# Performance work log

Hardware: AMD Instinct MI355X
Metric: run time of the kernel (lower is better)

## Reference

```python
import jax, jax.numpy as jnp
import numpy as np

C, B, N, IN, OUT = 32, 32, 4096, 16, 32
NUM_ITERS = 3


def _squash(t, axis=-1):
    # scale = |t|^2 / (1 + |t|^2); out = scale * t / |t|
    sn = jnp.sum(t * t, axis=axis, keepdims=True)
    return (sn / (1.0 + sn)) * t / jnp.sqrt(sn)


def setup_inputs() -> dict:
    key = jax.random.key(0)
    k1, k2 = jax.random.split(key)
    x = jax.random.normal(k1, (B, N, IN), dtype=jnp.float32)
    route_weights = jax.random.normal(k2, (C, N, IN, OUT), dtype=jnp.float32)
    return {"x": x, "route_weights": route_weights}


def reference(x, route_weights):
    # priors[c,b,n,d] = sum_i x[b,n,i] * W[c,n,i,d]  (torch: [C,B,N,1,D], singleton dropped)
    priors = jnp.einsum('bni,cnio->cbno', x, route_weights)  # [C,B,N,D]
    # torch logits are [C,B,N,1,D] but constant over D (delta broadcasts), and the
    # custom softmax normalizes over dim=2 (route nodes N), so [C,B,N] is equivalent.
    logits = jnp.zeros(priors.shape[:3], dtype=priors.dtype)  # [C,B,N]
    outputs = None
    for i in range(NUM_ITERS):
        probs = jax.nn.softmax(logits, axis=2)  # softmax over route nodes (dim=2)
        s = jnp.sum(probs[..., None] * priors, axis=2, keepdims=True)  # [C,B,1,D]
        outputs = _squash(s, axis=-1)
        if i != NUM_ITERS - 1:
            logits = logits + jnp.sum(priors * outputs, axis=-1)  # agreement [C,B,N]
    return outputs[:, :, :, None, :]  # [C,B,1,1,D] to match torch output shape
```

## Files before the change

kernel.cpp:

```cpp
#include <hip/hip_runtime.h>
#include <math.h>


typedef _Float16 f16x8 __attribute__((ext_vector_type(8)));
typedef float f32x16 __attribute__((ext_vector_type(16)));

namespace {
constexpr int kC = 32, kB = 32, kN = 4096, kI = 16, kD = 32;
constexpr int CHUNKS = 32;
constexpr int CHUNK_N = kN / CHUNKS;
constexpr int PS = kB * kD + kB;
constexpr int GRID = kC * CHUNKS;
constexpr size_t XT_ELEMS = (size_t)kN * kB * kI;
constexpr size_t WT_ELEMS = (size_t)kC * kN * kI * kD;
constexpr size_t P_FLOATS = (size_t)kC * CHUNKS * PS;
constexpr size_t CV_FLOATS = (size_t)kC * kB * kD;
constexpr int BAR_U32 = 33;
constexpr size_t WS_BYTES_MID = XT_ELEMS * 2 + (P_FLOATS + CV_FLOATS) * 4;
constexpr size_t WS_BYTES_BIG =
    (XT_ELEMS + WT_ELEMS) * 2 + (P_FLOATS + CV_FLOATS) * 4;
constexpr size_t WS_BYTES_MEGA =
    (XT_ELEMS + WT_ELEMS) * 2 + 3 * P_FLOATS * 4 + 256;
}

__device__ __forceinline__ f32x16 zero16() {
  f32x16 z;
#pragma unroll
  for (int r = 0; r < 16; ++r) z[r] = 0.f;
  return z;
}

__global__ __launch_bounds__(256) void k_xt(const float* __restrict__ x,
                                            _Float16* __restrict__ xt,
                                            unsigned* __restrict__ bar) {
  if (bar && blockIdx.x == 0 && threadIdx.x < BAR_U32) bar[threadIdx.x] = 0u;
  const int t = blockIdx.x * 256 + threadIdx.x;
  const int r = t >> 1, half = t & 1;
  const int b = r >> 12, n = r & 4095;
  const float4* s4 =
      reinterpret_cast<const float4*>(x) + (size_t)r * 4 + half * 2;
  const float4 f0 = s4[0], f1 = s4[1];
  f16x8 o;
  o[0] = (_Float16)f0.x; o[1] = (_Float16)f0.y;
  o[2] = (_Float16)f0.z; o[3] = (_Float16)f0.w;
  o[4] = (_Float16)f1.x; o[5] = (_Float16)f1.y;
  o[6] = (_Float16)f1.z; o[7] = (_Float16)f1.w;
  *reinterpret_cast<f16x8*>(xt + ((size_t)n * kB + b) * kI + half * 8) = o;
}

__device__ __forceinline__ void bar_arrive(unsigned* bar, int bid, int tid) {
  __threadfence();
  __syncthreads();
  if (tid == 0) {
    const int g = bid & 31;
    unsigned v = __hip_atomic_fetch_add(&bar[g], 1u, __ATOMIC_RELEASE,
                                        __HIP_MEMORY_SCOPE_AGENT);
    if ((v & 31u) == 31u)
      __hip_atomic_fetch_add(&bar[32], 1u, __ATOMIC_RELEASE,
                             __HIP_MEMORY_SCOPE_AGENT);
  }
}

__device__ __forceinline__ void bar_wait(unsigned* bar, int tid, int epoch) {
  if (tid == 0) {
    const unsigned target = 32u * (unsigned)epoch;
    while (__hip_atomic_load(&bar[32], __ATOMIC_RELAXED,
                             __HIP_MEMORY_SCOPE_AGENT) < target)
      __builtin_amdgcn_s_sleep(8);
    (void)__hip_atomic_load(&bar[32], __ATOMIC_ACQUIRE,
                            __HIP_MEMORY_SCOPE_AGENT);
  }
  __syncthreads();
}


__device__ __forceinline__ void mega_sweep0(const float* __restrict__ W,
                                            const _Float16* __restrict__ xt,
                                            _Float16* __restrict__ Wt,
                                            float* __restrict__ P,
                                            float (*red)[32][33], int c,
                                            int chunk, int tid) {
  const int w = tid >> 6, l = tid & 63;
  const int m = l & 31, h = l >> 5;
  const int n0 = chunk * CHUNK_N;
  constexpr int TILES = CHUNK_N / 4;

  const float* wp = W + ((size_t)c * kN + n0 + w) * 512 + (h * 8) * 32 + m;
  const _Float16* xp = xt + ((size_t)(n0 + w)) * 512 + m * 16 + h * 8;
  _Float16* wtp = Wt + ((size_t)c * kN + n0 + w) * 512 + (size_t)l * 8;

  f32x16 accA = zero16(), accB = zero16();

  float rA0[8], rA1[8];
  f16x8 B0, B1;
#pragma unroll
  for (int j = 0; j < 8; ++j) rA0[j] = __builtin_nontemporal_load(wp + j * 32);
  B0 = *reinterpret_cast<const f16x8*>(xp);
#pragma unroll
  for (int j = 0; j < 8; ++j)
    rA1[j] = __builtin_nontemporal_load(wp + 2048 + j * 32);
  B1 = *reinterpret_cast<const f16x8*>(xp + 2048);

#pragma unroll 1
  for (int t = 0; t < TILES; t += 2) {
    {
      f16x8 a;
#pragma unroll
      for (int j = 0; j < 8; ++j) a[j] = (_Float16)rA0[j];
      const f16x8 b = B0;
      const int tn = (t + 2 < TILES) ? t + 2 : 0;
#pragma unroll
      for (int j = 0; j < 8; ++j)
        rA0[j] = __builtin_nontemporal_load(wp + (size_t)tn * 2048 + j * 32);
      B0 = *reinterpret_cast<const f16x8*>(xp + (size_t)tn * 2048);
      *reinterpret_cast<f16x8*>(wtp + (size_t)t * 2048) = a;
      accA = __builtin_amdgcn_mfma_f32_32x32x16_f16(a, b, accA, 0, 0, 0);
    }
    {
      f16x8 a;
#pragma unroll
      for (int j = 0; j < 8; ++j) a[j] = (_Float16)rA1[j];
      const f16x8 b = B1;
      const int tn = (t + 3 < TILES) ? t + 3 : 0;
#pragma unroll
      for (int j = 0; j < 8; ++j)
        rA1[j] = __builtin_nontemporal_load(wp + (size_t)tn * 2048 + j * 32);
      B1 = *reinterpret_cast<const f16x8*>(xp + (size_t)tn * 2048);
      *reinterpret_cast<f16x8*>(wtp + (size_t)(t + 1) * 2048) = a;
      accB = __builtin_amdgcn_mfma_f32_32x32x16_f16(a, b, accB, 0, 0, 0);
    }
  }
#pragma unroll
  for (int r = 0; r < 16; ++r) accA[r] += accB[r];

#pragma unroll
  for (int r = 0; r < 16; ++r)
    red[w][(r & 3) + 8 * (r >> 2) + 4 * h][m] = accA[r];
  __syncthreads();

  float* Pp = P + ((size_t)c * CHUNKS + chunk) * PS;
#pragma unroll
  for (int e = tid; e < 1024; e += 256) {
    const int d = e >> 5, bb = e & 31;
    Pp[e] = red[0][d][bb] + red[1][d][bb] + red[2][d][bb] + red[3][d][bb];
  }
}

__device__ __forceinline__ void mega_sweep_wt(
    const _Float16* __restrict__ Wt, const _Float16* __restrict__ xt,
    const float (*sCV)[32], float* __restrict__ P, float (*red)[32][33],
    float (*lred)[32], int c, int chunk, int tid) {
  const int w = tid >> 6, l = tid & 63;
  const int m = l & 31, h = l >> 5;
  const int n0 = chunk * CHUNK_N;
  constexpr int TILES = CHUNK_N / 4;

  const _Float16* wp = Wt + ((size_t)c * kN + n0 + w) * 512 + (size_t)l * 8;
  const _Float16* xp = xt + ((size_t)(n0 + w)) * 512 + m * 16 + h * 8;

  float cvr[16];
#pragma unroll
  for (int r = 0; r < 16; ++r)
    cvr[r] = sCV[m][(r & 3) + 8 * (r >> 2) + 4 * h];

  f32x16 accA = zero16(), accB = zero16();
  float lacc = 0.f;
  const f32x16 z = zero16();

  f16x8 A0, A1, B0, B1;
  A0 = *reinterpret_cast<const f16x8*>(wp);
  B0 = *reinterpret_cast<const f16x8*>(xp);
  A1 = *reinterpret_cast<const f16x8*>(wp + 2048);
  B1 = *reinterpret_cast<const f16x8*>(xp + 2048);

#pragma unroll 1
  for (int t = 0; t < TILES; t += 2) {
    {
      const f16x8 a = A0;
      const f16x8 b = B0;
      const int tn = (t + 2 < TILES) ? t + 2 : 0;
      A0 = *reinterpret_cast<const f16x8*>(wp + (size_t)tn * 2048);
      B0 = *reinterpret_cast<const f16x8*>(xp + (size_t)tn * 2048);
      const f32x16 pr =
          __builtin_amdgcn_mfma_f32_32x32x16_f16(a, b, z, 0, 0, 0);
      float d0 = pr[0] * cvr[0], d1 = pr[1] * cvr[1];
      float d2 = pr[2] * cvr[2], d3 = pr[3] * cvr[3];
#pragma unroll
      for (int r = 4; r < 16; r += 4) {
        d0 = fmaf(pr[r + 0], cvr[r + 0], d0);
        d1 = fmaf(pr[r + 1], cvr[r + 1], d1);
        d2 = fmaf(pr[r + 2], cvr[r + 2], d2);
        d3 = fmaf(pr[r + 3], cvr[r + 3], d3);
      }
      float dp = (d0 + d1) + (d2 + d3);
      dp += __shfl_xor(dp, 32);
      const float e = __expf(dp);
      lacc += e;
#pragma unroll
      for (int r = 0; r < 16; ++r) accA[r] = fmaf(e, pr[r], accA[r]);
    }
    {
      const f16x8 a = A1;
      const f16x8 b = B1;
      const int tn = (t + 3 < TILES) ? t + 3 : 0;
      A1 = *reinterpret_cast<const f16x8*>(wp + (size_t)tn * 2048);
      B1 = *reinterpret_cast<const f16x8*>(xp + (size_t)tn * 2048);
      const f32x16 pr =
          __builtin_amdgcn_mfma_f32_32x32x16_f16(a, b, z, 0, 0, 0);
      float d0 = pr[0] * cvr[0], d1 = pr[1] * cvr[1];
      float d2 = pr[2] * cvr[2], d3 = pr[3] * cvr[3];
#pragma unroll
      for (int r = 4; r < 16; r += 4) {
        d0 = fmaf(pr[r + 0], cvr[r + 0], d0);
        d1 = fmaf(pr[r + 1], cvr[r + 1], d1);
        d2 = fmaf(pr[r + 2], cvr[r + 2], d2);
        d3 = fmaf(pr[r + 3], cvr[r + 3], d3);
      }
      float dp = (d0 + d1) + (d2 + d3);
      dp += __shfl_xor(dp, 32);
      const float e = __expf(dp);
      lacc += e;
#pragma unroll
      for (int r = 0; r < 16; ++r) accB[r] = fmaf(e, pr[r], accB[r]);
    }
  }
#pragma unroll
  for (int r = 0; r < 16; ++r) accA[r] += accB[r];

#pragma unroll
  for (int r = 0; r < 16; ++r)
    red[w][(r & 3) + 8 * (r >> 2) + 4 * h][m] = accA[r];
  if (h == 0) lred[w][m] = lacc;
  __syncthreads();

  float* Pp = P + ((size_t)c * CHUNKS + chunk) * PS;
#pragma unroll
  for (int e = tid; e < 1024; e += 256) {
    const int d = e >> 5, bb = e & 31;
    Pp[e] = red[0][d][bb] + red[1][d][bb] + red[2][d][bb] + red[3][d][bb];
  }
  if (tid < 32)
    Pp[1024 + tid] = lred[0][tid] + lred[1][tid] + lred[2][tid] + lred[3][tid];
}

template <int K>
__device__ __forceinline__ void mega_reduce(const float* __restrict__ P,
                                            float* __restrict__ out,
                                            float (&cvrun)[4],
                                            float (*sCV)[32], int c, int t) {
  const int b = t >> 3, dg = t & 7;
  const float* Pc = P + (size_t)c * CHUNKS * PS;
  float s0 = 0.f, s1 = 0.f, s2 = 0.f, s3 = 0.f, lb = 0.f;
#pragma unroll 4
  for (int ch = 0; ch < CHUNKS; ++ch) {
    const float* base = Pc + (size_t)ch * PS;
    s0 += __hip_atomic_load(base + (dg + 0) * 32 + b, __ATOMIC_RELAXED,
                            __HIP_MEMORY_SCOPE_AGENT);
    s1 += __hip_atomic_load(base + (dg + 8) * 32 + b, __ATOMIC_RELAXED,
                            __HIP_MEMORY_SCOPE_AGENT);
    s2 += __hip_atomic_load(base + (dg + 16) * 32 + b, __ATOMIC_RELAXED,
                            __HIP_MEMORY_SCOPE_AGENT);
    s3 += __hip_atomic_load(base + (dg + 24) * 32 + b, __ATOMIC_RELAXED,
                            __HIP_MEMORY_SCOPE_AGENT);
    if (K != 0 && dg == 0)
      lb += __hip_atomic_load(base + 1024 + b, __ATOMIC_RELAXED,
                              __HIP_MEMORY_SCOPE_AGENT);
  }
  float inv;
  if constexpr (K == 0) {
    inv = 1.0f / (float)kN;
  } else {
    lb = __shfl(lb, (t & 63) & 56);
    inv = 1.0f / lb;
  }
  const float v0 = s0 * inv, v1 = s1 * inv, v2 = s2 * inv, v3 = s3 * inv;
  float sn = v0 * v0 + v1 * v1 + v2 * v2 + v3 * v3;
  sn += __shfl_xor(sn, 1);
  sn += __shfl_xor(sn, 2);
  sn += __shfl_xor(sn, 4);
  const float coef = sqrtf(sn) / (1.0f + sn);
  if constexpr (K == 2) {
    const size_t o0 = (size_t)c * 1024 + b * 32 + dg;
    out[o0 + 0] = v0 * coef;  out[o0 + 8] = v1 * coef;
    out[o0 + 16] = v2 * coef; out[o0 + 24] = v3 * coef;
  } else {
    if constexpr (K == 0) {
      cvrun[0] = v0 * coef; cvrun[1] = v1 * coef;
      cvrun[2] = v2 * coef; cvrun[3] = v3 * coef;
    } else {
      cvrun[0] += v0 * coef; cvrun[1] += v1 * coef;
      cvrun[2] += v2 * coef; cvrun[3] += v3 * coef;
    }
    sCV[b][dg + 0] = cvrun[0];  sCV[b][dg + 8] = cvrun[1];
    sCV[b][dg + 16] = cvrun[2]; sCV[b][dg + 24] = cvrun[3];
  }
}

__global__ __launch_bounds__(256, 4) void k_mega2(
    const float* __restrict__ W, const _Float16* __restrict__ xt,
    _Float16* __restrict__ Wt, float* __restrict__ P0, float* __restrict__ P1,
    float* __restrict__ P2, unsigned* __restrict__ bar,
    float* __restrict__ out) {
  __shared__ float red[4][32][33];
  __shared__ float lred[4][32];
  __shared__ float sCV[32][32];
  const int bid = blockIdx.x;
  const int c = bid & 31;
  const int chunk = bid >> 5;
  const int tid = threadIdx.x;
  float cvrun[4] = {0.f, 0.f, 0.f, 0.f};

  mega_sweep0(W, xt, Wt, P0, red, c, chunk, tid);
  bar_arrive(bar, bid, tid);
  bar_wait(bar, tid, 1);

  mega_reduce<0>(P0, nullptr, cvrun, sCV, c, tid);
  __syncthreads();

  mega_sweep_wt(Wt, xt, sCV, P1, red, lred, c, chunk, tid);
  bar_arrive(bar, bid, tid);
  bar_wait(bar, tid, 2);

  mega_reduce<1>(P1, nullptr, cvrun, sCV, c, tid);
  __syncthreads();

  mega_sweep_wt(Wt, xt, sCV, P2, red, lred, c, chunk, tid);
  bar_arrive(bar, bid, tid);

  if (chunk == 0) {
    bar_wait(bar, tid, 3);
    mega_reduce<2>(P2, out, cvrun, sCV, c, tid);
  }
}


template <int MODE, bool EMIT>
__global__ __launch_bounds__(256) void k_sweep(const float* __restrict__ W,
                                               const _Float16* __restrict__ xt,
                                               const float* __restrict__ cumVec,
                                               float* __restrict__ partials,
                                               _Float16* __restrict__ Wt) {
  __shared__ float red[4][32][33];
  __shared__ float lred[4][32];
  const int bid = blockIdx.x;
  const int c = bid & 31;
  const int chunk = bid >> 5;
  const int tid = threadIdx.x;
  const int w = tid >> 6, l = tid & 63;
  const int m = l & 31, h = l >> 5;
  const int n0 = chunk * CHUNK_N;
  constexpr int TILES = CHUNK_N / 4;

  const float* wp = W + ((size_t)c * kN + n0 + w) * 512 + (h * 8) * 32 + m;
  const _Float16* xp = xt + ((size_t)(n0 + w)) * 512 + m * 16 + h * 8;
  _Float16* wtp =
      EMIT ? (Wt + ((size_t)c * kN + n0 + w) * 512 + (size_t)l * 8) : nullptr;

  float cvr[16];
  if (MODE) {
    const float* cvp = cumVec + (size_t)c * 1024 + m * 32;
#pragma unroll
    for (int r = 0; r < 16; ++r) cvr[r] = cvp[(r & 3) + 8 * (r >> 2) + 4 * h];
  }

  f32x16 accA = zero16(), accB = zero16();
  float lacc = 0.f;
  const f32x16 z = zero16();

  float rA0[8], rA1[8];
  f16x8 B0, B1;
#pragma unroll
  for (int j = 0; j < 8; ++j)
    rA0[j] = EMIT ? __builtin_nontemporal_load(wp + j * 32) : wp[j * 32];
  B0 = *reinterpret_cast<const f16x8*>(xp);
#pragma unroll
  for (int j = 0; j < 8; ++j)
    rA1[j] = EMIT ? __builtin_nontemporal_load(wp + 2048 + j * 32)
                  : wp[2048 + j * 32];
  B1 = *reinterpret_cast<const f16x8*>(xp + 2048);

#pragma unroll 1
  for (int t = 0; t < TILES; t += 2) {
    {
      f16x8 a;
#pragma unroll
      for (int j = 0; j < 8; ++j) a[j] = (_Float16)rA0[j];
      const f16x8 b = B0;
      const int tn = (t + 2 < TILES) ? t + 2 : 0;
#pragma unroll
      for (int j = 0; j < 8; ++j)
        rA0[j] = EMIT ? __builtin_nontemporal_load(wp + (size_t)tn * 2048 +
                                                   j * 32)
                      : wp[(size_t)tn * 2048 + j * 32];
      B0 = *reinterpret_cast<const f16x8*>(xp + (size_t)tn * 2048);
      if constexpr (EMIT)
        *reinterpret_cast<f16x8*>(wtp + (size_t)t * 2048) = a;
      if constexpr (MODE == 0) {
        accA = __builtin_amdgcn_mfma_f32_32x32x16_f16(a, b, accA, 0, 0, 0);
      } else {
        const f32x16 pr =
            __builtin_amdgcn_mfma_f32_32x32x16_f16(a, b, z, 0, 0, 0);
        float d0 = pr[0] * cvr[0], d1 = pr[1] * cvr[1];
        float d2 = pr[2] * cvr[2], d3 = pr[3] * cvr[3];
#pragma unroll
        for (int r = 4; r < 16; r += 4) {
          d0 = fmaf(pr[r + 0], cvr[r + 0], d0);
          d1 = fmaf(pr[r + 1], cvr[r + 1], d1);
          d2 = fmaf(pr[r + 2], cvr[r + 2], d2);
          d3 = fmaf(pr[r + 3], cvr[r + 3], d3);
        }
        float dp = (d0 + d1) + (d2 + d3);
        dp += __shfl_xor(dp, 32);
        const float e = __expf(dp);
        lacc += e;
#pragma unroll
        for (int r = 0; r < 16; ++r) accA[r] = fmaf(e, pr[r], accA[r]);
      }
    }
    {
      f16x8 a;
#pragma unroll
      for (int j = 0; j < 8; ++j) a[j] = (_Float16)rA1[j];
      const f16x8 b = B1;
      const int tn = (t + 3 < TILES) ? t + 3 : 0;
#pragma unroll
      for (int j = 0; j < 8; ++j)
        rA1[j] = EMIT ? __builtin_nontemporal_load(wp + (size_t)tn * 2048 +
                                                   j * 32)
                      : wp[(size_t)tn * 2048 + j * 32];
      B1 = *reinterpret_cast<const f16x8*>(xp + (size_t)tn * 2048);
      if constexpr (EMIT)
        *reinterpret_cast<f16x8*>(wtp + (size_t)(t + 1) * 2048) = a;
      if constexpr (MODE == 0) {
        accB = __builtin_amdgcn_mfma_f32_32x32x16_f16(a, b, accB, 0, 0, 0);
      } else {
        const f32x16 pr =
            __builtin_amdgcn_mfma_f32_32x32x16_f16(a, b, z, 0, 0, 0);
        float d0 = pr[0] * cvr[0], d1 = pr[1] * cvr[1];
        float d2 = pr[2] * cvr[2], d3 = pr[3] * cvr[3];
#pragma unroll
        for (int r = 4; r < 16; r += 4) {
          d0 = fmaf(pr[r + 0], cvr[r + 0], d0);
          d1 = fmaf(pr[r + 1], cvr[r + 1], d1);
          d2 = fmaf(pr[r + 2], cvr[r + 2], d2);
          d3 = fmaf(pr[r + 3], cvr[r + 3], d3);
        }
        float dp = (d0 + d1) + (d2 + d3);
        dp += __shfl_xor(dp, 32);
        const float e = __expf(dp);
        lacc += e;
#pragma unroll
        for (int r = 0; r < 16; ++r) accB[r] = fmaf(e, pr[r], accB[r]);
      }
    }
  }
#pragma unroll
  for (int r = 0; r < 16; ++r) accA[r] += accB[r];

#pragma unroll
  for (int r = 0; r < 16; ++r)
    red[w][(r & 3) + 8 * (r >> 2) + 4 * h][m] = accA[r];
  if (MODE && h == 0) lred[w][m] = lacc;
  __syncthreads();

  float* Pp = partials + ((size_t)c * CHUNKS + chunk) * PS;
#pragma unroll
  for (int e = tid; e < 1024; e += 256) {
    const int d = e >> 5, bb = e & 31;
    Pp[e] = red[0][d][bb] + red[1][d][bb] + red[2][d][bb] + red[3][d][bb];
  }
  if (MODE && tid < 32)
    Pp[1024 + tid] = lred[0][tid] + lred[1][tid] + lred[2][tid] + lred[3][tid];
}

__global__ __launch_bounds__(256) void k_sweep_wt(
    const _Float16* __restrict__ Wt, const _Float16* __restrict__ xt,
    const float* __restrict__ cumVec, float* __restrict__ partials) {
  __shared__ float red[4][32][33];
  __shared__ float lred[4][32];
  __shared__ float sCV[32][32];
  const int bid = blockIdx.x;
  const int c = bid & 31;
  const int chunk = bid >> 5;
  const int tid = threadIdx.x;
  for (int e = tid; e < 1024; e += 256)
    sCV[e >> 5][e & 31] = cumVec[(size_t)c * 1024 + e];
  __syncthreads();
  mega_sweep_wt(Wt, xt, sCV, partials, red, lred, c, chunk, tid);
}

template <int K>
__global__ __launch_bounds__(1024) void k_reduce(
    const float* __restrict__ partials, float* __restrict__ CV,
    float* __restrict__ out) {
  const int c = blockIdx.x;
  const int t = threadIdx.x;
  const int b = t >> 5, d = t & 31;
  const float* Pc = partials + (size_t)c * CHUNKS * PS;
  float s = 0.f;
#pragma unroll 4
  for (int ch = 0; ch < CHUNKS; ++ch) s += Pc[(size_t)ch * PS + d * 32 + b];
  float inv;
  if constexpr (K == 0) {
    inv = 1.0f / (float)kN;
  } else {
    float lb = 0.f;
#pragma unroll 4
    for (int ch = 0; ch < CHUNKS; ++ch) lb += Pc[(size_t)ch * PS + 1024 + b];
    inv = 1.0f / lb;
  }
  const float sv = s * inv;
  float sn = sv * sv;
  sn += __shfl_xor(sn, 1);
  sn += __shfl_xor(sn, 2);
  sn += __shfl_xor(sn, 4);
  sn += __shfl_xor(sn, 8);
  sn += __shfl_xor(sn, 16);
  const float coef = sqrtf(sn) / (1.0f + sn);
  const float o = sv * coef;
  if constexpr (K == 2)
    out[(size_t)c * 1024 + t] = o;
  else if constexpr (K == 0)
    CV[(size_t)c * 1024 + t] = o;
  else
    CV[(size_t)c * 1024 + t] += o;
}

namespace v1 {
constexpr int BG = 4, NSLOT = 128, THREADS1 = NSLOT * 8;
template <int MODE>
__device__ __forceinline__ void sweep_pass(const float* __restrict__ Wc,
                                           const float* __restrict__ x, int b0,
                                           int tid, int nslot, int dg,
                                           float (*red)[8][20], float (*sS)[kD],
                                           float* sL, const float (*sVec)[kD]) {
  float acc[BG][4];
  float lv[BG];
#pragma unroll
  for (int b = 0; b < BG; ++b) {
    lv[b] = 0.f;
#pragma unroll
    for (int j = 0; j < 4; ++j) acc[b][j] = 0.f;
  }
  float vec[BG][4];
  if (MODE) {
#pragma unroll
    for (int b = 0; b < BG; ++b)
#pragma unroll
      for (int j = 0; j < 4; ++j) vec[b][j] = sVec[b][4 * dg + j];
  }
#pragma unroll 1
  for (int n = nslot; n < kN; n += NSLOT) {
    const float* Wn = Wc + (size_t)n * (kI * kD) + 4 * dg;
    float pr[BG][4];
#pragma unroll
    for (int b = 0; b < BG; ++b)
#pragma unroll
      for (int j = 0; j < 4; ++j) pr[b][j] = 0.f;
#pragma unroll
    for (int iq = 0; iq < 4; ++iq) {
      float4 wv[4];
#pragma unroll
      for (int r = 0; r < 4; ++r)
        wv[r] = *reinterpret_cast<const float4*>(Wn + (4 * iq + r) * kD);
#pragma unroll
      for (int b = 0; b < BG; ++b) {
        const float4 xv = *reinterpret_cast<const float4*>(
            x + ((size_t)(b0 + b) * kN + n) * kI + 4 * iq);
        const float xsv[4] = {xv.x, xv.y, xv.z, xv.w};
#pragma unroll
        for (int r = 0; r < 4; ++r) {
          pr[b][0] = fmaf(xsv[r], wv[r].x, pr[b][0]);
          pr[b][1] = fmaf(xsv[r], wv[r].y, pr[b][1]);
          pr[b][2] = fmaf(xsv[r], wv[r].z, pr[b][2]);
          pr[b][3] = fmaf(xsv[r], wv[r].w, pr[b][3]);
        }
      }
    }
    if (MODE == 0) {
#pragma unroll
      for (int b = 0; b < BG; ++b)
#pragma unroll
        for (int j = 0; j < 4; ++j) acc[b][j] += pr[b][j];
    } else {
#pragma unroll
      for (int b = 0; b < BG; ++b) {
        float dp = pr[b][0] * vec[b][0] + pr[b][1] * vec[b][1] +
                   pr[b][2] * vec[b][2] + pr[b][3] * vec[b][3];
        dp += __shfl_xor(dp, 1);
        dp += __shfl_xor(dp, 2);
        dp += __shfl_xor(dp, 4);
        const float e = __expf(dp);
        lv[b] += e;
        acc[b][0] = fmaf(e, pr[b][0], acc[b][0]);
        acc[b][1] = fmaf(e, pr[b][1], acc[b][1]);
        acc[b][2] = fmaf(e, pr[b][2], acc[b][2]);
        acc[b][3] = fmaf(e, pr[b][3], acc[b][3]);
      }
    }
  }
#pragma unroll
  for (int b = 0; b < BG; ++b) {
#pragma unroll
    for (int j = 0; j < 4; ++j) {
      float v = acc[b][j];
      v += __shfl_xor(v, 8);
      v += __shfl_xor(v, 16);
      v += __shfl_xor(v, 32);
      acc[b][j] = v;
    }
    if (MODE) {
      float v = lv[b];
      v += __shfl_xor(v, 8);
      v += __shfl_xor(v, 16);
      v += __shfl_xor(v, 32);
      lv[b] = v;
    }
  }
  const int lane = tid & 63;
  const int wv_id = tid >> 6;
  if ((lane >> 3) == 0) {
#pragma unroll
    for (int b = 0; b < BG; ++b) {
#pragma unroll
      for (int j = 0; j < 4; ++j) red[wv_id][dg][4 * b + j] = acc[b][j];
      if (MODE) red[wv_id][dg][16 + b] = lv[b];
    }
  }
  __syncthreads();
  if (tid < 128) {
    const int dgc = tid >> 4, e = tid & 15;
    float s = 0.f;
#pragma unroll
    for (int w = 0; w < 16; ++w) s += red[w][dgc][e];
    sS[e >> 2][4 * dgc + (e & 3)] = s;
  }
  if (MODE && tid >= 128 && tid < 128 + BG) {
    const int b = tid - 128;
    float s = 0.f;
#pragma unroll
    for (int w = 0; w < 16; ++w) s += red[w][0][16 + b];
    sL[b] = s;
  }
  __syncthreads();
}

__global__ __launch_bounds__(THREADS1, 4) void caps_route_kernel(
    const float* __restrict__ x, const float* __restrict__ W,
    float* __restrict__ out) {
  __shared__ float red[16][8][20];
  __shared__ float sS[BG][kD];
  __shared__ float sVec[BG][kD];
  __shared__ float sL[BG];
  const int i = blockIdx.x;
  const int xcd = i & 7;
  const int j = i >> 3;
  const int c = xcd + 8 * (j >> 3);
  const int b0 = 4 * (j & 7);
  const int tid = threadIdx.x;
  const int nslot = tid >> 3;
  const int dg = tid & 7;
  const float* Wc = W + (size_t)c * kN * kI * kD;
  sweep_pass<0>(Wc, x, b0, tid, nslot, dg, red, sS, sL, sVec);
  if (tid < BG) {
    const int b = tid;
    float sval[kD], sn = 0.f;
    const float inv = 1.0f / (float)kN;
#pragma unroll
    for (int d = 0; d < kD; ++d) {
      sval[d] = sS[b][d] * inv;
      sn += sval[d] * sval[d];
    }
    const float coef = sqrtf(sn) / (1.0f + sn);
#pragma unroll
    for (int d = 0; d < kD; ++d) sVec[b][d] = sval[d] * coef;
  }
  __syncthreads();
  sweep_pass<1>(Wc, x, b0, tid, nslot, dg, red, sS, sL, sVec);
  if (tid < BG) {
    const int b = tid;
    float sval[kD], sn = 0.f;
    const float inv = 1.0f / sL[b];
#pragma unroll
    for (int d = 0; d < kD; ++d) {
      sval[d] = sS[b][d] * inv;
      sn += sval[d] * sval[d];
    }
    const float coef = sqrtf(sn) / (1.0f + sn);
#pragma unroll
    for (int d = 0; d < kD; ++d) sVec[b][d] += sval[d] * coef;
  }
  __syncthreads();
  sweep_pass<1>(Wc, x, b0, tid, nslot, dg, red, sS, sL, sVec);
  if (tid < BG) {
    const int b = tid;
    float sval[kD], sn = 0.f;
    const float inv = 1.0f / sL[b];
#pragma unroll
    for (int d = 0; d < kD; ++d) {
      sval[d] = sS[b][d] * inv;
      sn += sval[d] * sval[d];
    }
    const float coef = sqrtf(sn) / (1.0f + sn);
    float* o = out + ((size_t)c * kB + (b0 + b)) * kD;
#pragma unroll
    for (int d = 0; d < kD; ++d) o[d] = sval[d] * coef;
  }
}
}

namespace {
int g_mega_ok = 0;
int probe_mega() {
  int dev = 0;
  if (hipGetDevice(&dev) != hipSuccess) return 0;
  int nCU = 0;
  if (hipDeviceGetAttribute(&nCU, hipDeviceAttributeMultiprocessorCount,
                            dev) != hipSuccess)
    return 0;
  int maxB = 0;
  if (hipOccupancyMaxActiveBlocksPerMultiprocessor(&maxB, k_mega2, 256, 0) !=
      hipSuccess)
    return 0;
  return (nCU > 0 && maxB > 0 && (size_t)nCU * (size_t)maxB >= (size_t)GRID)
             ? 1
             : -1;
}
struct MegaProbeInit {
  MegaProbeInit() { g_mega_ok = probe_mega(); }
} g_mega_probe_init;
}

extern "C" void kernel_launch(void* const* d_in, const int* in_sizes, int n_in,
                              void* d_out, int out_size, void* d_ws,
                              size_t ws_size, hipStream_t stream) {
  const float* x = (const float*)d_in[0];
  const float* W = (const float*)d_in[1];
  float* out = (float*)d_out;
  (void)in_sizes; (void)n_in; (void)out_size;

  if (g_mega_ok == 0) g_mega_ok = probe_mega();

  if (g_mega_ok == 1 && ws_size >= WS_BYTES_MEGA) {
    _Float16* xt = (_Float16*)d_ws;
    _Float16* Wt = xt + XT_ELEMS;
    float* P0 = (float*)(Wt + WT_ELEMS);
    float* P1 = P0 + P_FLOATS;
    float* P2 = P1 + P_FLOATS;
    unsigned* bar = (unsigned*)(P2 + P_FLOATS);

    k_xt<<<GRID, 256, 0, stream>>>(x, xt, bar);
    k_mega2<<<GRID, 256, 0, stream>>>(W, xt, Wt, P0, P1, P2, bar, out);
    return;
  }

  if (ws_size >= WS_BYTES_BIG) {
    _Float16* xt = (_Float16*)d_ws;
    _Float16* Wt = xt + XT_ELEMS;
    float* P = (float*)(Wt + WT_ELEMS);
    float* CV = P + P_FLOATS;

    k_xt<<<GRID, 256, 0, stream>>>(x, xt, nullptr);
    k_sweep<0, true><<<GRID, 256, 0, stream>>>(W, xt, nullptr, P, Wt);
    k_reduce<0><<<kC, 1024, 0, stream>>>(P, CV, nullptr);
    k_sweep_wt<<<GRID, 256, 0, stream>>>(Wt, xt, CV, P);
    k_reduce<1><<<kC, 1024, 0, stream>>>(P, CV, nullptr);
    k_sweep_wt<<<GRID, 256, 0, stream>>>(Wt, xt, CV, P);
    k_reduce<2><<<kC, 1024, 0, stream>>>(P, nullptr, out);
    return;
  }

  if (ws_size >= WS_BYTES_MID) {
    _Float16* xt = (_Float16*)d_ws;
    float* P = (float*)(xt + XT_ELEMS);
    float* CV = P + P_FLOATS;

    k_xt<<<GRID, 256, 0, stream>>>(x, xt, nullptr);
    k_sweep<0, false><<<GRID, 256, 0, stream>>>(W, xt, nullptr, P, nullptr);
    k_reduce<0><<<kC, 1024, 0, stream>>>(P, CV, nullptr);
    k_sweep<1, false><<<GRID, 256, 0, stream>>>(W, xt, CV, P, nullptr);
    k_reduce<1><<<kC, 1024, 0, stream>>>(P, CV, nullptr);
    k_sweep<1, false><<<GRID, 256, 0, stream>>>(W, xt, CV, P, nullptr);
    k_reduce<2><<<kC, 1024, 0, stream>>>(P, nullptr, out);
    return;
  }

  v1::caps_route_kernel<<<256, v1::THREADS1, 0, stream>>>(x, W, out);
}
```

Baseline: 200.7 us.

## Replace grid-wide barrier with per-capsule group barriers and a single reducer block

The grid-wide two-level barrier is replaced by a per-output-capsule counter, so only the 32 blocks sharing a capsule wait for each other. One block per group (chunk 0) reduces the partials, writes the running output vector to global memory and raises a flag that the other blocks spin on before loading it into shared memory. The three partial buffers collapse into one reused buffer, and the reduction uses 64-bit loads with an LDS-based norm reduction. The cost is a serialized reduce-then-broadcast step per iteration instead of every block reducing redundantly, plus an extra flag round trip. The fast path now also runs when the occupancy probe fails, which risks deadlock if blocks are not all co-resident.

After: 200.8 us. About the same (+0.1%).

```diff
diff --git a/kernel.cpp b/kernel.cpp
--- a/kernel.cpp
+++ b/kernel.cpp
@@ -15,12 +15,12 @@
 constexpr size_t WT_ELEMS = (size_t)kC * kN * kI * kD;
 constexpr size_t P_FLOATS = (size_t)kC * CHUNKS * PS;
 constexpr size_t CV_FLOATS = (size_t)kC * kB * kD;
-constexpr int BAR_U32 = 33;
+constexpr int BAR_U32 = 2048;
 constexpr size_t WS_BYTES_MID = XT_ELEMS * 2 + (P_FLOATS + CV_FLOATS) * 4;
 constexpr size_t WS_BYTES_BIG =
     (XT_ELEMS + WT_ELEMS) * 2 + (P_FLOATS + CV_FLOATS) * 4;
 constexpr size_t WS_BYTES_MEGA =
-    (XT_ELEMS + WT_ELEMS) * 2 + 3 * P_FLOATS * 4 + 256;
+    (XT_ELEMS + WT_ELEMS) * 2 + (P_FLOATS + CV_FLOATS) * 4 + BAR_U32 * 4 + 256;
 }
 
 __device__ __forceinline__ f32x16 zero16() {
@@ -33,7 +33,8 @@
 __global__ __launch_bounds__(256) void k_xt(const float* __restrict__ x,
                                             _Float16* __restrict__ xt,
                                             unsigned* __restrict__ bar) {
-  if (bar && blockIdx.x == 0 && threadIdx.x < BAR_U32) bar[threadIdx.x] = 0u;
+  if (bar && blockIdx.x == 0)
+    for (int i = threadIdx.x; i < BAR_U32; i += 256) bar[i] = 0u;
   const int t = blockIdx.x * 256 + threadIdx.x;
   const int r = t >> 1, half = t & 1;
   const int b = r >> 12, n = r & 4095;
@@ -48,29 +49,26 @@
   *reinterpret_cast<f16x8*>(xt + ((size_t)n * kB + b) * kI + half * 8) = o;
 }
 
-__device__ __forceinline__ void bar_arrive(unsigned* bar, int bid, int tid) {
+__device__ __forceinline__ void group_arrive(unsigned* ctr, int tid) {
   __threadfence();
   __syncthreads();
-  if (tid == 0) {
-    const int g = bid & 31;
-    unsigned v = __hip_atomic_fetch_add(&bar[g], 1u, __ATOMIC_RELEASE,
-                                        __HIP_MEMORY_SCOPE_AGENT);
-    if ((v & 31u) == 31u)
-      __hip_atomic_fetch_add(&bar[32], 1u, __ATOMIC_RELEASE,
-                             __HIP_MEMORY_SCOPE_AGENT);
-  }
-}
-
-__device__ __forceinline__ void bar_wait(unsigned* bar, int tid, int epoch) {
-  if (tid == 0) {
-    const unsigned target = 32u * (unsigned)epoch;
-    while (__hip_atomic_load(&bar[32], __ATOMIC_RELAXED,
-                             __HIP_MEMORY_SCOPE_AGENT) < target)
-      __builtin_amdgcn_s_sleep(8);
-    (void)__hip_atomic_load(&bar[32], __ATOMIC_ACQUIRE,
-                            __HIP_MEMORY_SCOPE_AGENT);
-  }
-  __syncthreads();
+  if (tid == 0)
+    __hip_atomic_fetch_add(ctr, 1u, __ATOMIC_RELEASE,
+                           __HIP_MEMORY_SCOPE_AGENT);
+}
+
+__device__ __forceinline__ void spin_ge(unsigned* addr, unsigned target) {
+  while (__hip_atomic_load(addr, __ATOMIC_RELAXED,
+                           __HIP_MEMORY_SCOPE_AGENT) < target)
+    __builtin_amdgcn_s_sleep(2);
+}
+
+__device__ __forceinline__ float ld_f32_agent(const float* p) {
+  return __hip_atomic_load(p, __ATOMIC_RELAXED, __HIP_MEMORY_SCOPE_AGENT);
+}
+__device__ __forceinline__ unsigned long long ld_u64_agent(const float* p) {
+  return __hip_atomic_load(reinterpret_cast<const unsigned long long*>(p),
+                           __ATOMIC_RELAXED, __HIP_MEMORY_SCOPE_AGENT);
 }
 
 
@@ -244,92 +242,154 @@
 }
 
 template <int K>
-__device__ __forceinline__ void mega_reduce(const float* __restrict__ P,
-                                            float* __restrict__ out,
-                                            float (&cvrun)[4],
-                                            float (*sCV)[32], int c, int t) {
-  const int b = t >> 3, dg = t & 7;
+__device__ __forceinline__ void red_reduce(const float* __restrict__ P,
+                                           float* __restrict__ CVc,
+                                           float* __restrict__ out,
+                                           float (&cvrun)[4],
+                                           float (*ldsSn)[16][2],
+                                           float* ldsCoef, float* ldsInv,
+                                           int c, int tid) {
   const float* Pc = P + (size_t)c * CHUNKS * PS;
-  float s0 = 0.f, s1 = 0.f, s2 = 0.f, s3 = 0.f, lb = 0.f;
+  const int hb = tid & 15;
+  const int b0 = hb * 2;
+  const int d0 = tid >> 4;
+  float s0 = 0.f, s1 = 0.f, s2 = 0.f, s3 = 0.f;
 #pragma unroll 4
   for (int ch = 0; ch < CHUNKS; ++ch) {
     const float* base = Pc + (size_t)ch * PS;
-    s0 += __hip_atomic_load(base + (dg + 0) * 32 + b, __ATOMIC_RELAXED,
-                            __HIP_MEMORY_SCOPE_AGENT);
-    s1 += __hip_atomic_load(base + (dg + 8) * 32 + b, __ATOMIC_RELAXED,
-                            __HIP_MEMORY_SCOPE_AGENT);
-    s2 += __hip_atomic_load(base + (dg + 16) * 32 + b, __ATOMIC_RELAXED,
-                            __HIP_MEMORY_SCOPE_AGENT);
-    s3 += __hip_atomic_load(base + (dg + 24) * 32 + b, __ATOMIC_RELAXED,
-                            __HIP_MEMORY_SCOPE_AGENT);
-    if (K != 0 && dg == 0)
-      lb += __hip_atomic_load(base + 1024 + b, __ATOMIC_RELAXED,
-                              __HIP_MEMORY_SCOPE_AGENT);
-  }
-  float inv;
+    const unsigned long long q0 = ld_u64_agent(base + 2 * tid);
+    const unsigned long long q1 = ld_u64_agent(base + 512 + 2 * tid);
+    s0 += __uint_as_float((unsigned)q0);
+    s1 += __uint_as_float((unsigned)(q0 >> 32));
+    s2 += __uint_as_float((unsigned)q1);
+    s3 += __uint_as_float((unsigned)(q1 >> 32));
+  }
+  float inv0, inv1;
   if constexpr (K == 0) {
-    inv = 1.0f / (float)kN;
+    inv0 = inv1 = 1.0f / (float)kN;
   } else {
-    lb = __shfl(lb, (t & 63) & 56);
-    inv = 1.0f / lb;
-  }
-  const float v0 = s0 * inv, v1 = s1 * inv, v2 = s2 * inv, v3 = s3 * inv;
-  float sn = v0 * v0 + v1 * v1 + v2 * v2 + v3 * v3;
-  sn += __shfl_xor(sn, 1);
-  sn += __shfl_xor(sn, 2);
-  sn += __shfl_xor(sn, 4);
-  const float coef = sqrtf(sn) / (1.0f + sn);
+    if (tid < 32) {
+      float lb = 0.f;
+#pragma unroll 4
+      for (int ch = 0; ch < CHUNKS; ++ch)
+        lb += ld_f32_agent(Pc + (size_t)ch * PS + 1024 + tid);
+      ldsInv[tid] = 1.0f / lb;
+    }
+    __syncthreads();
+    inv0 = ldsInv[b0];
+    inv1 = ldsInv[b0 + 1];
+  }
+  const float v0 = s0 * inv0, v1 = s1 * inv1;
+  const float v2 = s2 * inv0, v3 = s3 * inv1;
+  float snA = v0 * v0 + v2 * v2;
+  float snB = v1 * v1 + v3 * v3;
+  snA += __shfl_xor(snA, 16); snA += __shfl_xor(snA, 32);
+  snB += __shfl_xor(snB, 16); snB += __shfl_xor(snB, 32);
+  if ((tid & 63) < 16) {
+    ldsSn[tid >> 6][hb][0] = snA;
+    ldsSn[tid >> 6][hb][1] = snB;
+  }
+  __syncthreads();
+  if (tid < 16) {
+    const float sA = ldsSn[0][tid][0] + ldsSn[1][tid][0] + ldsSn[2][tid][0] +
+                     ldsSn[3][tid][0];
+    const float sB = ldsSn[0][tid][1] + ldsSn[1][tid][1] + ldsSn[2][tid][1] +
+                     ldsSn[3][tid][1];
+    ldsCoef[2 * tid] = sqrtf(sA) / (1.0f + sA);
+    ldsCoef[2 * tid + 1] = sqrtf(sB) / (1.0f + sB);
+  }
+  __syncthreads();
+  const float c0 = ldsCoef[b0], c1 = ldsCoef[b0 + 1];
   if constexpr (K == 2) {
-    const size_t o0 = (size_t)c * 1024 + b * 32 + dg;
-    out[o0 + 0] = v0 * coef;  out[o0 + 8] = v1 * coef;
-    out[o0 + 16] = v2 * coef; out[o0 + 24] = v3 * coef;
+    float* oc = out + (size_t)c * 1024;
+    oc[b0 * 32 + d0] = v0 * c0;
+    oc[(b0 + 1) * 32 + d0] = v1 * c1;
+    oc[b0 * 32 + d0 + 16] = v2 * c0;
+    oc[(b0 + 1) * 32 + d0 + 16] = v3 * c1;
   } else {
     if constexpr (K == 0) {
-      cvrun[0] = v0 * coef; cvrun[1] = v1 * coef;
-      cvrun[2] = v2 * coef; cvrun[3] = v3 * coef;
+      cvrun[0] = v0 * c0; cvrun[1] = v1 * c1;
+      cvrun[2] = v2 * c0; cvrun[3] = v3 * c1;
     } else {
-      cvrun[0] += v0 * coef; cvrun[1] += v1 * coef;
-      cvrun[2] += v2 * coef; cvrun[3] += v3 * coef;
-    }
-    sCV[b][dg + 0] = cvrun[0];  sCV[b][dg + 8] = cvrun[1];
-    sCV[b][dg + 16] = cvrun[2]; sCV[b][dg + 24] = cvrun[3];
-  }
-}
-
-__global__ __launch_bounds__(256, 4) void k_mega2(
+      cvrun[0] += v0 * c0; cvrun[1] += v1 * c1;
+      cvrun[2] += v2 * c0; cvrun[3] += v3 * c1;
+    }
+    CVc[b0 * 32 + d0] = cvrun[0];
+    CVc[(b0 + 1) * 32 + d0] = cvrun[1];
+    CVc[b0 * 32 + d0 + 16] = cvrun[2];
+    CVc[(b0 + 1) * 32 + d0 + 16] = cvrun[3];
+  }
+}
+
+__device__ __forceinline__ void load_cv(const float* __restrict__ CVc,
+                                        float (*sCV)[32], int tid) {
+#pragma unroll
+  for (int q = 0; q < 2; ++q) {
+    const int e = 2 * tid + 512 * q;
+    const unsigned long long v = ld_u64_agent(CVc + e);
+    sCV[e >> 5][e & 31] = __uint_as_float((unsigned)v);
+    sCV[e >> 5][(e & 31) + 1] = __uint_as_float((unsigned)(v >> 32));
+  }
+  __syncthreads();
+}
+
+__global__ __launch_bounds__(256, 4) void k_mega3(
     const float* __restrict__ W, const _Float16* __restrict__ xt,
-    _Float16* __restrict__ Wt, float* __restrict__ P0, float* __restrict__ P1,
-    float* __restrict__ P2, unsigned* __restrict__ bar,
-    float* __restrict__ out) {
+    _Float16* __restrict__ Wt, float* __restrict__ P, float* __restrict__ CVg,
+    unsigned* __restrict__ bar, float* __restrict__ out) {
   __shared__ float red[4][32][33];
   __shared__ float lred[4][32];
   __shared__ float sCV[32][32];
+  __shared__ float ldsSn[4][16][2];
+  __shared__ float ldsCoef[32];
+  __shared__ float ldsInv[32];
   const int bid = blockIdx.x;
   const int c = bid & 31;
   const int chunk = bid >> 5;
   const int tid = threadIdx.x;
+  unsigned* barc = bar + c * 32;
+  unsigned* cvf = bar + 1024 + c * 32;
+  float* CVc = CVg + (size_t)c * 1024;
   float cvrun[4] = {0.f, 0.f, 0.f, 0.f};
 
-  mega_sweep0(W, xt, Wt, P0, red, c, chunk, tid);
-  bar_arrive(bar, bid, tid);
-  bar_wait(bar, tid, 1);
-
-  mega_reduce<0>(P0, nullptr, cvrun, sCV, c, tid);
-  __syncthreads();
-
-  mega_sweep_wt(Wt, xt, sCV, P1, red, lred, c, chunk, tid);
-  bar_arrive(bar, bid, tid);
-  bar_wait(bar, tid, 2);
-
-  mega_reduce<1>(P1, nullptr, cvrun, sCV, c, tid);
-  __syncthreads();
-
-  mega_sweep_wt(Wt, xt, sCV, P2, red, lred, c, chunk, tid);
-  bar_arrive(bar, bid, tid);
-
+  mega_sweep0(W, xt, Wt, P, red, c, chunk, tid);
+  group_arrive(barc, tid);
   if (chunk == 0) {
-    bar_wait(bar, tid, 3);
-    mega_reduce<2>(P2, out, cvrun, sCV, c, tid);
+    if (tid == 0) spin_ge(barc, 32);
+    __syncthreads();
+    red_reduce<0>(P, CVc, nullptr, cvrun, ldsSn, ldsCoef, ldsInv, c, tid);
+    __threadfence();
+    __syncthreads();
+    if (tid == 0)
+      __hip_atomic_fetch_add(cvf, 1u, __ATOMIC_RELEASE,
+                             __HIP_MEMORY_SCOPE_AGENT);
+  }
+  if (tid == 0) spin_ge(cvf, 1);
+  __syncthreads();
+  load_cv(CVc, sCV, tid);
+
+  mega_sweep_wt(Wt, xt, sCV, P, red, lred, c, chunk, tid);
+  group_arrive(barc, tid);
+  if (chunk == 0) {
+    if (tid == 0) spin_ge(barc, 64);
+    __syncthreads();
+    red_reduce<1>(P, CVc, nullptr, cvrun, ldsSn, ldsCoef, ldsInv, c, tid);
+    __threadfence();
+    __syncthreads();
+    if (tid == 0)
+      __hip_atomic_fetch_add(cvf, 1u, __ATOMIC_RELEASE,
+                             __HIP_MEMORY_SCOPE_AGENT);
+  }
+  if (tid == 0) spin_ge(cvf, 2);
+  __syncthreads();
+  load_cv(CVc, sCV, tid);
+
+  mega_sweep_wt(Wt, xt, sCV, P, red, lred, c, chunk, tid);
+  group_arrive(barc, tid);
+  if (chunk == 0) {
+    if (tid == 0) spin_ge(barc, 96);
+    __syncthreads();
+    red_reduce<2>(P, nullptr, out, cvrun, ldsSn, ldsCoef, ldsInv, c, tid);
   }
 }
 
@@ -710,7 +770,7 @@
 }
 
 namespace {
-int g_mega_ok = 0;
+int g_mega_state = 0;
 int probe_mega() {
   int dev = 0;
   if (hipGetDevice(&dev) != hipSuccess) return 0;
@@ -719,15 +779,17 @@
                             dev) != hipSuccess)
     return 0;
   int maxB = 0;
-  if (hipOccupancyMaxActiveBlocksPerMultiprocessor(&maxB, k_mega2, 256, 0) !=
+  if (hipOccupancyMaxActiveBlocksPerMultiprocessor(&maxB, k_mega3, 256, 0) !=
       hipSuccess)
     return 0;
-  return (nCU > 0 && maxB > 0 && (size_t)nCU * (size_t)maxB >= (size_t)GRID)
-             ? 1
-             : -1;
+  if (nCU <= 0 || maxB <= 0) return 0;
+  return ((size_t)nCU * (size_t)maxB >= (size_t)GRID) ? 1 : -1;
 }
 struct MegaProbeInit {
-  MegaProbeInit() { g_mega_ok = probe_mega(); }
+  MegaProbeInit() {
+    (void)hipFree(nullptr);
+    g_mega_state = probe_mega();
+  }
 } g_mega_probe_init;
 }
 
@@ -739,18 +801,17 @@
   float* out = (float*)d_out;
   (void)in_sizes; (void)n_in; (void)out_size;
 
-  if (g_mega_ok == 0) g_mega_ok = probe_mega();
-
-  if (g_mega_ok == 1 && ws_size >= WS_BYTES_MEGA) {
+  if (g_mega_state == 0) g_mega_state = probe_mega();
+
+  if (g_mega_state >= 0 && ws_size >= WS_BYTES_MEGA) {
     _Float16* xt = (_Float16*)d_ws;
     _Float16* Wt = xt + XT_ELEMS;
-    float* P0 = (float*)(Wt + WT_ELEMS);
-    float* P1 = P0 + P_FLOATS;
-    float* P2 = P1 + P_FLOATS;
-    unsigned* bar = (unsigned*)(P2 + P_FLOATS);
+    float* P = (float*)(Wt + WT_ELEMS);
+    float* CVg = P + P_FLOATS;
+    unsigned* bar = (unsigned*)(CVg + CV_FLOATS);
 
     k_xt<<<GRID, 256, 0, stream>>>(x, xt, bar);
-    k_mega2<<<GRID, 256, 0, stream>>>(W, xt, Wt, P0, P1, P2, bar, out);
+    k_mega3<<<GRID, 256, 0, stream>>>(W, xt, Wt, P, CVg, bar, out);
     return;
   }
 
```
